# Optimization experiments

Hardware: AMD Instinct MI355X
Metric: run time of the kernel (lower is better)

## Reference

```python
import jax, jax.numpy as jnp
import numpy as np

K = 31  # AvgPool2d kernel size
P = 15  # padding


def _box_avg(x):
    """31x31 stride-1 avg pool, count_include_pad=True (PyTorch default):
    separable ones-conv with zero padding, divided by K*K."""
    B, C, H, W = x.shape
    kh = jnp.ones((C, 1, K, 1), x.dtype)
    kw = jnp.ones((C, 1, 1, K), x.dtype)
    dn = ('NCHW', 'OIHW', 'NCHW')
    y = jax.lax.conv_general_dilated(x, kh, (1, 1), [(P, P), (0, 0)],
                                     dimension_numbers=dn, feature_group_count=C)
    y = jax.lax.conv_general_dilated(y, kw, (1, 1), [(0, 0), (P, P)],
                                     dimension_numbers=dn, feature_group_count=C)
    return y / (K * K)


def setup_inputs() -> dict:
    key = jax.random.key(0)
    k1, k2 = jax.random.split(key)
    pred = jax.random.normal(k1, (64, 1, 512, 512), dtype=jnp.float32)
    mask = jax.random.uniform(k2, (64, 1, 512, 512), dtype=jnp.float32)
    return {"pred": pred, "mask": mask}


def reference(pred, mask):
    weit = 1.0 + 5.0 * jnp.abs(_box_avg(mask) - mask)
    p = jax.nn.sigmoid(pred)
    inter = jnp.sum(p * mask * weit, axis=(2, 3))          # [B, C]
    union = jnp.sum((p + mask) * weit, axis=(2, 3))        # [B, C]
    wdiss = 1.0 - (2.0 * inter + 0.5) / (union + 0.5)
    return jnp.mean(wdiss)
```

## Files before the change

### kernel.cpp

```cpp
#include <hip/hip_runtime.h>
#include <hip/hip_bf16.h>
#include <math.h>

#define NB 64
#define HH 512
#define WW 512
#define KK 31
#define PP 15
#define NSTRIP 16
#define SROWS (HH / NSTRIP)
#define RPB 4
#define NROUND (SROWS / RPB)
#define PSTR 544


__global__ __launch_bounds__(512, 8) void dice_strip_kernel(
        const float* __restrict__ pred,
        const float* __restrict__ mask,
        float* __restrict__ part) {
    const int strip = blockIdx.x;
    const int b     = blockIdx.y;
    const int x     = threadIdx.x;
    const int wave  = x >> 6;
    const int lane  = x & 63;

    __shared__ float wtot[RPB * 8];
    __shared__ float Pbuf[RPB * PSTR];
    __shared__ float red[16];

    const float* mbase = mask + (size_t)b * HH * WW;
    const float* pbase = pred + (size_t)b * HH * WW;
    const int y0 = strip * SROWS;

    if (x < 16) {
        #pragma unroll
        for (int r = 0; r < RPB; ++r) Pbuf[r * PSTR + x] = 0.0f;
    }

    float vcarry = 0.0f;
    {
        const int rlo = (y0 - PP - 1 < 0) ? 0 : y0 - PP - 1;
        const int rhi = (y0 + PP - 1 > HH - 1) ? HH - 1 : y0 + PP - 1;
        for (int r = rlo; r <= rhi; ++r) vcarry += mbase[r * WW + x];
    }

    float inter = 0.0f, uni = 0.0f;

    for (int j = 0; j < NROUND; ++j) {
        const int y = y0 + j * RPB;

        float en[RPB], lv[RPB], mc[RPB], pv[RPB];
        #pragma unroll
        for (int r = 0; r < RPB; ++r) {
            const int ra = y + r + PP;
            const int rs = y + r - PP - 1;
            en[r] = (ra < HH) ? mbase[ra * WW + x] : 0.0f;
            lv[r] = (rs >= 0) ? mbase[rs * WW + x] : 0.0f;
            mc[r] = mbase[(y + r) * WW + x];
            pv[r] = pbase[(y + r) * WW + x];
        }

        float incl[RPB];
        {
            float run = vcarry;
            #pragma unroll
            for (int r = 0; r < RPB; ++r) {
                run += en[r] - lv[r];
                incl[r] = run;
            }
            vcarry = run;
        }

        #pragma unroll
        for (int off = 1; off < 64; off <<= 1) {
            float t[RPB];
            #pragma unroll
            for (int r = 0; r < RPB; ++r) t[r] = __shfl_up(incl[r], off);
            #pragma unroll
            for (int r = 0; r < RPB; ++r) if (lane >= off) incl[r] += t[r];
        }

        if (lane == 63) {
            #pragma unroll
            for (int r = 0; r < RPB; ++r) wtot[r * 8 + wave] = incl[r];
        }
        __syncthreads();

        float bm[RPB];
        #pragma unroll
        for (int r = 0; r < RPB; ++r)
            bm[r] = (lane < wave) ? wtot[r * 8 + lane] : 0.0f;
        #pragma unroll
        for (int off = 1; off < 64; off <<= 1) {
            #pragma unroll
            for (int r = 0; r < RPB; ++r) bm[r] += __shfl_xor(bm[r], off);
        }

        #pragma unroll
        for (int r = 0; r < RPB; ++r) Pbuf[r * PSTR + 16 + x] = bm[r] + incl[r];
        if (wave == 7) {
            #pragma unroll
            for (int r = 0; r < RPB; ++r) {
                const float p511 = bm[r] + wtot[r * 8 + 7];
                if (lane >= 48) Pbuf[r * PSTR + 528 + (lane - 48)] = p511;
            }
        }
        __syncthreads();

        #pragma unroll
        for (int r = 0; r < RPB; ++r) {
            const float hsum = Pbuf[r * PSTR + 16 + x + PP] - Pbuf[r * PSTR + x];
            const float avg  = hsum * (1.0f / (float)(KK * KK));
            const float m    = mc[r];
            const float w    = 1.0f + 5.0f * fabsf(avg - m);
            const float sg   = 1.0f / (1.0f + __expf(-pv[r]));
            inter += sg * m * w;
            uni   += (sg + m) * w;
        }
    }

    #pragma unroll
    for (int off = 32; off > 0; off >>= 1) {
        inter += __shfl_down(inter, off);
        uni   += __shfl_down(uni, off);
    }
    if (lane == 0) { red[wave] = inter; red[8 + wave] = uni; }
    __syncthreads();
    if (x == 0) {
        float ti = 0.0f, tu = 0.0f;
        #pragma unroll
        for (int w2 = 0; w2 < 8; ++w2) { ti += red[w2]; tu += red[8 + w2]; }
        const int bid = b * NSTRIP + strip;
        part[bid] = ti;
        part[NB * NSTRIP + bid] = tu;
    }
}

__global__ void dice_final_kernel(const float* __restrict__ part,
                                  float* __restrict__ out) {
    const int t = threadIdx.x;
    float inter = 0.0f, uni = 0.0f;
    #pragma unroll
    for (int s = 0; s < NSTRIP; ++s) {
        inter += part[t * NSTRIP + s];
        uni   += part[NB * NSTRIP + t * NSTRIP + s];
    }
    float wd = 1.0f - (2.0f * inter + 0.5f) / (uni + 0.5f);
    #pragma unroll
    for (int off = 32; off > 0; off >>= 1) wd += __shfl_down(wd, off);
    if (t == 0) out[0] = wd * (1.0f / (float)NB);
}

extern "C" void kernel_launch(void* const* d_in, const int* in_sizes, int n_in,
                              void* d_out, int out_size, void* d_ws, size_t ws_size,
                              hipStream_t stream) {
    const float* pred = (const float*)d_in[0];
    const float* mask = (const float*)d_in[1];
    float* out  = (float*)d_out;
    float* part = (float*)d_ws;

    dim3 grid(NSTRIP, NB);
    dice_strip_kernel<<<grid, 512, 0, stream>>>(pred, mask, part);
    dice_final_kernel<<<1, 64, 0, stream>>>(part, out);
}
```

Before: 180.0 us.

## Split box filter into horizontal-sum pass and vertical sliding-window pass

Adds a first kernel that computes the 31-wide horizontal box sums of each mask row with a wave-level prefix scan and writes them to a workspace buffer. A second kernel then runs a per-column vertical sliding window over those sums and accumulates the dice terms. This removes the per-round block-wide scans and barriers of the fused strip kernel. In exchange it writes and rereads a full-size intermediate buffer, adding global memory traffic. The old fused kernel remains as a fallback when the workspace is too small.

```diff
diff --git a/kernel.cpp b/kernel.cpp
--- a/kernel.cpp
+++ b/kernel.cpp
@@ -9,10 +9,140 @@
 #define PP 15
 #define NSTRIP 16
 #define SROWS (HH / NSTRIP)
+#define NROWS (NB * HH)
+#define ROWS_PER_WAVE 8
+
+#define WS_NEED (8192 + (size_t)NROWS * WW * 4)
+
+__global__ __launch_bounds__(256) void hrow_kernel(const float* __restrict__ mask,
+                                                   float* __restrict__ H) {
+    const int gw   = (blockIdx.x * 256 + threadIdx.x) >> 6;
+    const int lane = threadIdx.x & 63;
+
+    for (int k = 0; k < ROWS_PER_WAVE; ++k) {
+        const size_t r = (size_t)gw * ROWS_PER_WAVE + k;
+        const float* row = mask + r * WW;
+        const int xbase = lane * 8;
+        const float4 a = *(const float4*)(row + xbase);
+        const float4 b = *(const float4*)(row + xbase + 4);
+
+        float s0 = a.x;
+        float s1 = s0 + a.y;
+        float s2 = s1 + a.z;
+        float s3 = s2 + a.w;
+        float s4 = s3 + b.x;
+        float s5 = s4 + b.y;
+        float s6 = s5 + b.z;
+        float s7 = s6 + b.w;
+
+        float incl = s7;
+        #pragma unroll
+        for (int off = 1; off < 64; off <<= 1) {
+            float t = __shfl_up(incl, off);
+            if (lane >= off) incl += t;
+        }
+        const float base = incl - s7;
+        s0 += base; s1 += base; s2 += base; s3 += base;
+        s4 += base; s5 += base; s6 += base; s7 += base;
+
+        const float total = __shfl(incl, 63);
+
+        float hi0 = __shfl_down(s7, 1);
+        float hi1 = __shfl_down(s0, 2);
+        float hi2 = __shfl_down(s1, 2);
+        float hi3 = __shfl_down(s2, 2);
+        float hi4 = __shfl_down(s3, 2);
+        float hi5 = __shfl_down(s4, 2);
+        float hi6 = __shfl_down(s5, 2);
+        float hi7 = __shfl_down(s6, 2);
+        float lo0 = __shfl_up(s0, 2);
+        float lo1 = __shfl_up(s1, 2);
+        float lo2 = __shfl_up(s2, 2);
+        float lo3 = __shfl_up(s3, 2);
+        float lo4 = __shfl_up(s4, 2);
+        float lo5 = __shfl_up(s5, 2);
+        float lo6 = __shfl_up(s6, 2);
+        float lo7 = __shfl_up(s7, 2);
+
+        float h[8];
+        const float hiv[8] = {hi0, hi1, hi2, hi3, hi4, hi5, hi6, hi7};
+        const float lov[8] = {lo0, lo1, lo2, lo3, lo4, lo5, lo6, lo7};
+        #pragma unroll
+        for (int j = 0; j < 8; ++j) {
+            const int x = xbase + j;
+            const float mhi = (x + PP > WW - 1) ? total : hiv[j];
+            const float mlo = (x - PP - 1 >= 0) ? lov[j] : 0.0f;
+            h[j] = mhi - mlo;
+        }
+
+        float* orow = H + r * WW;
+        *(float4*)(orow + xbase)     = make_float4(h[0], h[1], h[2], h[3]);
+        *(float4*)(orow + xbase + 4) = make_float4(h[4], h[5], h[6], h[7]);
+    }
+}
+
+__global__ __launch_bounds__(512) void dice_kernel(
+        const float* __restrict__ pred,
+        const float* __restrict__ mask,
+        const float* __restrict__ H,
+        float* __restrict__ part) {
+    const int strip = blockIdx.x;
+    const int b     = blockIdx.y;
+    const int x     = threadIdx.x;
+    const int wave  = x >> 6;
+    const int lane  = x & 63;
+
+    __shared__ float red[16];
+
+    const float* Hb = H    + (size_t)b * HH * WW;
+    const float* mb = mask + (size_t)b * HH * WW;
+    const float* pb = pred + (size_t)b * HH * WW;
+    const int y0 = strip * SROWS;
+
+    float B = 0.0f;
+    {
+        const int rlo = (y0 - PP < 0) ? 0 : y0 - PP;
+        const int rhi = y0 + PP - 1;
+        for (int r = rlo; r <= rhi; ++r) B += Hb[r * WW + x];
+    }
+
+    float inter = 0.0f, uni = 0.0f;
+    #pragma unroll 4
+    for (int i = 0; i < SROWS; ++i) {
+        const int y = y0 + i;
+        const float he = (y + PP < HH) ? Hb[(y + PP) * WW + x] : 0.0f;
+        const float hl = (y - PP >= 0) ? Hb[(y - PP) * WW + x] : 0.0f;
+        const float m  = mb[y * WW + x];
+        const float p  = pb[y * WW + x];
+        B += he;
+        const float avg = B * (1.0f / (float)(KK * KK));
+        const float w   = 1.0f + 5.0f * fabsf(avg - m);
+        const float sg  = 1.0f / (1.0f + __expf(-p));
+        inter += sg * m * w;
+        uni   += (sg + m) * w;
+        B -= hl;
+    }
+
+    #pragma unroll
+    for (int off = 32; off > 0; off >>= 1) {
+        inter += __shfl_down(inter, off);
+        uni   += __shfl_down(uni, off);
+    }
+    if (lane == 0) { red[wave] = inter; red[8 + wave] = uni; }
+    __syncthreads();
+    if (x == 0) {
+        float ti = 0.0f, tu = 0.0f;
+        #pragma unroll
+        for (int w2 = 0; w2 < 8; ++w2) { ti += red[w2]; tu += red[8 + w2]; }
+        const int bid = b * NSTRIP + strip;
+        part[bid] = ti;
+        part[NB * NSTRIP + bid] = tu;
+    }
+}
+
 #define RPB 4
 #define NROUND (SROWS / RPB)
 #define PSTR 544
-
 
 __global__ __launch_bounds__(512, 8) void dice_strip_kernel(
         const float* __restrict__ pred,
@@ -48,7 +178,6 @@
 
     for (int j = 0; j < NROUND; ++j) {
         const int y = y0 + j * RPB;
-
         float en[RPB], lv[RPB], mc[RPB], pv[RPB];
         #pragma unroll
         for (int r = 0; r < RPB; ++r) {
@@ -59,18 +188,13 @@
             mc[r] = mbase[(y + r) * WW + x];
             pv[r] = pbase[(y + r) * WW + x];
         }
-
         float incl[RPB];
         {
             float run = vcarry;
             #pragma unroll
-            for (int r = 0; r < RPB; ++r) {
-                run += en[r] - lv[r];
-                incl[r] = run;
-            }
+            for (int r = 0; r < RPB; ++r) { run += en[r] - lv[r]; incl[r] = run; }
             vcarry = run;
         }
-
         #pragma unroll
         for (int off = 1; off < 64; off <<= 1) {
             float t[RPB];
@@ -79,23 +203,19 @@
             #pragma unroll
             for (int r = 0; r < RPB; ++r) if (lane >= off) incl[r] += t[r];
         }
-
         if (lane == 63) {
             #pragma unroll
             for (int r = 0; r < RPB; ++r) wtot[r * 8 + wave] = incl[r];
         }
         __syncthreads();
-
         float bm[RPB];
         #pragma unroll
-        for (int r = 0; r < RPB; ++r)
-            bm[r] = (lane < wave) ? wtot[r * 8 + lane] : 0.0f;
+        for (int r = 0; r < RPB; ++r) bm[r] = (lane < wave) ? wtot[r * 8 + lane] : 0.0f;
         #pragma unroll
         for (int off = 1; off < 64; off <<= 1) {
             #pragma unroll
             for (int r = 0; r < RPB; ++r) bm[r] += __shfl_xor(bm[r], off);
         }
-
         #pragma unroll
         for (int r = 0; r < RPB; ++r) Pbuf[r * PSTR + 16 + x] = bm[r] + incl[r];
         if (wave == 7) {
@@ -106,7 +226,6 @@
             }
         }
         __syncthreads();
-
         #pragma unroll
         for (int r = 0; r < RPB; ++r) {
             const float hsum = Pbuf[r * PSTR + 16 + x + PP] - Pbuf[r * PSTR + x];
@@ -158,8 +277,14 @@
     const float* mask = (const float*)d_in[1];
     float* out  = (float*)d_out;
     float* part = (float*)d_ws;
-
-    dim3 grid(NSTRIP, NB);
-    dice_strip_kernel<<<grid, 512, 0, stream>>>(pred, mask, part);
+    float* H    = (float*)((char*)d_ws + 8192);
+
+    dim3 grid2(NSTRIP, NB);
+    if (ws_size >= WS_NEED) {
+        hrow_kernel<<<1024, 256, 0, stream>>>(mask, H);
+        dice_kernel<<<grid2, 512, 0, stream>>>(pred, mask, H, part);
+    } else {
+        dice_strip_kernel<<<grid2, 512, 0, stream>>>(pred, mask, part);
+    }
     dice_final_kernel<<<1, 64, 0, stream>>>(part, out);
 }
```

New measurement: 180.7 us. About the same (+0.4%).
